# Kernel optimization log

Hardware: AMD Instinct MI355X
Metric: run time of the kernel (lower is better)

The kernel has to match this reference:

```python
import jax, jax.numpy as jnp
import numpy as np

B, T, D, H, HD = 4, 2048, 1024, 16, 64
EPS = 1e-6


def _rotary_tables(seq_len, d_head):
    n = d_head // 4
    angular_freq = (1.0 / 1024) ** jnp.linspace(0, 1, n, dtype=jnp.float32)
    angular_freq = jnp.concatenate([angular_freq, jnp.zeros((n,), jnp.float32)])  # [d_head//2]
    theta = jnp.outer(jnp.arange(seq_len, dtype=jnp.float32), angular_freq)  # [T, d_head//2]
    return jnp.cos(theta), jnp.sin(theta)


def _apply_rotary(x, cos, sin):
    # x: [B, T, H, d]
    xf = x.astype(jnp.float32)
    x1, x2 = jnp.split(xf, 2, axis=-1)
    c = cos[None, :, None, :]
    s = sin[None, :, None, :]
    y1 = x1 * c + x2 * s
    y2 = -x1 * s + x2 * c
    return jnp.concatenate([y1, y2], axis=-1).astype(x.dtype)


def _rmsnorm(x, eps):
    return x * jax.lax.rsqrt(jnp.mean(x * x, axis=-1, keepdims=True) + eps)


def setup_inputs() -> dict:
    key = jax.random.key(0)
    ks = jax.random.split(key, 5)
    scale = 1.0 / np.sqrt(D)
    x = jax.random.normal(ks[0], (B, T, D), jnp.float32)
    wq = jax.random.normal(ks[1], (D, D), jnp.float32) * scale
    wk = jax.random.normal(ks[2], (D, D), jnp.float32) * scale
    wv = jax.random.normal(ks[3], (D, D), jnp.float32) * scale
    wo = jax.random.normal(ks[4], (D, D), jnp.float32) * scale
    mask = jnp.tril(jnp.ones((T, T), dtype=bool))  # causal
    return {"x": x, "wq": wq, "wk": wk, "wv": wv, "wo": wo, "mask": mask}


def reference(x, wq, wk, wv, wo, mask):
    # QKV projections (equinox Linear: y = x @ W.T)
    q = (x @ wq.T).reshape(B, T, H, HD)
    k = (x @ wk.T).reshape(B, T, H, HD)
    v = (x @ wv.T).reshape(B, T, H, HD)
    # QK-norm (RMS norm without weight)
    q = _rmsnorm(q, EPS)
    k = _rmsnorm(k, EPS)
    # Rotary embedding
    cos, sin = _rotary_tables(T, HD)
    q = _apply_rotary(q, cos, sin)
    k = _apply_rotary(k, cos, sin)
    # Attention
    scores = jnp.einsum('bshd,bthd->bhst', q, k) / jnp.sqrt(jnp.float32(HD))
    scores = jnp.where(mask[None, None, :, :], scores, -jnp.inf)
    weights = jax.nn.softmax(scores, axis=-1)
    out = jnp.einsum('bhst,bthd->bshd', weights, v)
    out = out.reshape(B, T, D)
    return out @ wo.T
```

## Files before the change

### kernel.cpp

```cpp
#include <hip/hip_runtime.h>
#include <hip/hip_bf16.h>
#include <math.h>

#define B_ 4
#define T_ 2048
#define D_ 1024
#define H_ 16
#define HD_ 64

typedef _Float16 f16x8 __attribute__((ext_vector_type(8)));
typedef _Float16 f16x4 __attribute__((ext_vector_type(4)));
typedef float f32x4 __attribute__((ext_vector_type(4)));

__device__ __forceinline__ void gload_lds16(const _Float16* g, _Float16* l) {
    __builtin_amdgcn_global_load_lds(
        (const __attribute__((address_space(1))) void*)g,
        (__attribute__((address_space(3))) void*)l,
        16, 0, 0);
}

__global__ __launch_bounds__(256) void castall(const float* __restrict__ x,
                                               const float* __restrict__ wq,
                                               const float* __restrict__ wk,
                                               const float* __restrict__ wv,
                                               const float* __restrict__ wo,
                                               _Float16* __restrict__ xh,
                                               _Float16* __restrict__ wqh,
                                               _Float16* __restrict__ wkh,
                                               _Float16* __restrict__ wvh,
                                               _Float16* __restrict__ woh) {
    const int gi = blockIdx.x * 256 + threadIdx.x;
    const float* in;
    _Float16* out;
    int off;
    if (gi < (1 << 21)) {
        in = x; out = xh; off = gi;
    } else {
        const int j = gi - (1 << 21);
        const int w = j >> 18;
        off = j & ((1 << 18) - 1);
        in  = (w == 0) ? wq : (w == 1 ? wk : (w == 2 ? wv : wo));
        out = (w == 0) ? wqh : (w == 1 ? wkh : (w == 2 ? wvh : woh));
    }
    const float4 v = ((const float4*)in)[off];
    f16x4 h = {(_Float16)v.x, (_Float16)v.y, (_Float16)v.z, (_Float16)v.w};
    ((f16x4*)out)[off] = h;
}

__global__ __launch_bounds__(256) void gemm_qkv(const _Float16* __restrict__ A,
                                                const _Float16* __restrict__ Wq,
                                                const _Float16* __restrict__ Wk,
                                                const _Float16* __restrict__ Wv,
                                                _Float16* __restrict__ qh,
                                                _Float16* __restrict__ kh,
                                                _Float16* __restrict__ vt) {
    constexpr int K = D_;
    const int id  = blockIdx.x + 8 * (blockIdx.y + 64 * blockIdx.z);
    const int nid = (id & 7) * 192 + (id >> 3);
    const int bx  = nid & 7;
    const int rem = nid >> 3;
    const int by  = rem & 63;
    const int z   = rem >> 6;

    const _Float16* W = (z == 0) ? Wq : (z == 1 ? Wk : Wv);
    __shared__ _Float16 As[128 * 32];
    __shared__ _Float16 Bs[128 * 32];
    const int tid = threadIdx.x;
    const int lane = tid & 63, w = tid >> 6;
    const int col = lane & 15, quad = lane >> 4;
    const int wm = w >> 1, wn = w & 1;
    const int row0 = by * 128, col0 = bx * 128;
    const int sr = lane >> 2, sc = (lane & 3) * 8;

    f32x4 acc[4][4];
#pragma unroll
    for (int i = 0; i < 4; ++i)
#pragma unroll
        for (int j = 0; j < 4; ++j) acc[i][j] = (f32x4){0.f, 0.f, 0.f, 0.f};

    for (int kt = 0; kt < K / 32; ++kt) {
        const int k0 = kt * 32;
#pragma unroll
        for (int it = 0; it < 2; ++it) {
            const int rb = it * 64 + w * 16;
            gload_lds16(A + (size_t)(row0 + rb + sr) * K + k0 + sc, As + rb * 32);
            gload_lds16(W + (size_t)(col0 + rb + sr) * K + k0 + sc, Bs + rb * 32);
        }
        __syncthreads();
        f16x8 af[4], bf[4];
#pragma unroll
        for (int i = 0; i < 4; ++i) {
            af[i] = *(const f16x8*)&As[(wm * 64 + i * 16 + col) * 32 + quad * 8];
            bf[i] = *(const f16x8*)&Bs[(wn * 64 + i * 16 + col) * 32 + quad * 8];
        }
#pragma unroll
        for (int mi = 0; mi < 4; ++mi)
#pragma unroll
            for (int ni = 0; ni < 4; ++ni)
                acc[mi][ni] = __builtin_amdgcn_mfma_f32_16x16x32_f16(af[mi], bf[ni],
                                                                     acc[mi][ni], 0, 0, 0);
        __syncthreads();
    }

    if (z < 2) {
        _Float16* C = (z == 0) ? qh : kh;
        const float qscale = (z == 0) ? 0.18033688011112042f : 1.0f;
        const float fr = exp2f(-10.0f * (float)col * (1.0f / 15.0f));
#pragma unroll
        for (int mi = 0; mi < 4; ++mi) {
            float ssq[4];
#pragma unroll
            for (int r = 0; r < 4; ++r) {
                float t = 0.f;
#pragma unroll
                for (int ni = 0; ni < 4; ++ni) t += acc[mi][ni][r] * acc[mi][ni][r];
                ssq[r] = t;
            }
#pragma unroll
            for (int st = 1; st < 16; st <<= 1)
#pragma unroll
                for (int r = 0; r < 4; ++r) ssq[r] += __shfl_xor(ssq[r], st, 64);
            const int rowb = row0 + wm * 64 + mi * 16 + quad * 4;
#pragma unroll
            for (int r = 0; r < 4; ++r) {
                const float scl = rsqrtf(ssq[r] * (1.0f / 64.0f) + 1e-6f) * qscale;
                const int t = (rowb + r) & (T_ - 1);
                float s, c;
                sincosf((float)t * fr, &s, &c);
                const float x0 = acc[mi][0][r] * scl;
                const float x1 = acc[mi][1][r] * scl;
                const float x2 = acc[mi][2][r] * scl;
                const float x3 = acc[mi][3][r] * scl;
                const float y0 = fmaf(x0, c, x2 * s);
                const float y2 = fmaf(x2, c, -x0 * s);
                const size_t base = (size_t)(rowb + r) * D_ + col0 + wn * 64 + col;
                C[base + 0]  = (_Float16)y0;
                C[base + 16] = (_Float16)x1;
                C[base + 32] = (_Float16)y2;
                C[base + 48] = (_Float16)x3;
            }
        }
    } else {
        const int hh = bx * 2 + wn;
#pragma unroll
        for (int mi = 0; mi < 4; ++mi) {
            const int row = row0 + wm * 64 + mi * 16 + quad * 4;
            const int bb = row >> 11;
            const int t0m = row & (T_ - 1);
#pragma unroll
            for (int ni = 0; ni < 4; ++ni) {
                const int d = ni * 16 + col;
                f16x4 pk = {(_Float16)acc[mi][ni][0], (_Float16)acc[mi][ni][1],
                            (_Float16)acc[mi][ni][2], (_Float16)acc[mi][ni][3]};
                *(f16x4*)&vt[((size_t)(bb * H_ + hh) * HD_ + d) * T_ + t0m] = pk;
            }
        }
    }
}

__global__ __launch_bounds__(256) void gemm_wo(const _Float16* __restrict__ A,
                                               const _Float16* __restrict__ W,
                                               float* __restrict__ C) {
    constexpr int K = D_, N = D_;
    const int id  = blockIdx.x + 8 * blockIdx.y;
    const int nid = (id & 7) * 64 + (id >> 3);
    const int bx  = nid & 7;
    const int by  = nid >> 3;

    __shared__ _Float16 As[128 * 32];
    __shared__ _Float16 Bs[128 * 32];
    const int tid = threadIdx.x;
    const int lane = tid & 63, w = tid >> 6;
    const int col = lane & 15, quad = lane >> 4;
    const int wm = w >> 1, wn = w & 1;
    const int row0 = by * 128, col0 = bx * 128;
    const int sr = lane >> 2, sc = (lane & 3) * 8;

    f32x4 acc[4][4];
#pragma unroll
    for (int i = 0; i < 4; ++i)
#pragma unroll
        for (int j = 0; j < 4; ++j) acc[i][j] = (f32x4){0.f, 0.f, 0.f, 0.f};

    for (int kt = 0; kt < K / 32; ++kt) {
        const int k0 = kt * 32;
#pragma unroll
        for (int it = 0; it < 2; ++it) {
            const int rb = it * 64 + w * 16;
            gload_lds16(A + (size_t)(row0 + rb + sr) * K + k0 + sc, As + rb * 32);
            gload_lds16(W + (size_t)(col0 + rb + sr) * K + k0 + sc, Bs + rb * 32);
        }
        __syncthreads();
        f16x8 af[4], bf[4];
#pragma unroll
        for (int i = 0; i < 4; ++i) {
            af[i] = *(const f16x8*)&As[(wm * 64 + i * 16 + col) * 32 + quad * 8];
            bf[i] = *(const f16x8*)&Bs[(wn * 64 + i * 16 + col) * 32 + quad * 8];
        }
#pragma unroll
        for (int mi = 0; mi < 4; ++mi)
#pragma unroll
            for (int ni = 0; ni < 4; ++ni)
                acc[mi][ni] = __builtin_amdgcn_mfma_f32_16x16x32_f16(af[mi], bf[ni],
                                                                     acc[mi][ni], 0, 0, 0);
        __syncthreads();
    }
#pragma unroll
    for (int mi = 0; mi < 4; ++mi)
#pragma unroll
        for (int ni = 0; ni < 4; ++ni)
#pragma unroll
            for (int r = 0; r < 4; ++r)
                C[(size_t)(row0 + wm * 64 + mi * 16 + quad * 4 + r) * N +
                  col0 + wn * 64 + ni * 16 + col] = acc[mi][ni][r];
}

#define LDP 88

__global__ __launch_bounds__(512) void flash_mfma(const _Float16* __restrict__ qh,
                                                  const _Float16* __restrict__ kh,
                                                  const _Float16* __restrict__ vt,
                                                  _Float16* __restrict__ o) {
    __shared__ _Float16 Kl[2][64 * 64];
    __shared__ _Float16 Vl[2][64 * 64];
    __shared__ _Float16 Pl[8][16 * LDP];
    const int tid = threadIdx.x;
    const int lane = tid & 63, w = tid >> 6;
    const int col = lane & 15, quad = lane >> 4;
    const int bh = blockIdx.x, b = bh >> 4, h = bh & 15;
    const int srow = lane >> 3;
    const int schunk = (lane & 7) ^ srow;
    const int sw = col & 7;
    const int rstg = w * 8 + srow;

    const _Float16* kbase = kh + ((size_t)b * T_ * H_ + (size_t)h) * HD_;
    const _Float16* vbase = vt + ((size_t)(b * H_ + h)) * (size_t)HD_ * T_;

    for (int phase = 0; phase < 2; ++phase) {
        const int qt = (phase == 0) ? (int)blockIdx.y : (15 - (int)blockIdx.y);
        const int q0 = qt * 128;

        const int tq = q0 + w * 16 + col;
        const _Float16* qp = qh + ((size_t)(b * T_ + tq) * H_ + h) * HD_ + quad * 8;
        const f16x8 qB0 = *(const f16x8*)(qp);
        const f16x8 qB1 = *(const f16x8*)(qp + 32);

        f32x4 oa[4];
#pragma unroll
        for (int i = 0; i < 4; ++i) oa[i] = (f32x4){0.f, 0.f, 0.f, 0.f};
        float l_ = 0.f;

        const int nkt = 2 * qt + 2;

        gload_lds16(kbase + (size_t)(0 + rstg) * H_ * HD_ + schunk * 8,
                    &Kl[0][(w * 8) * 64]);
        gload_lds16(vbase + (size_t)rstg * T_ + 0 + schunk * 8,
                    &Vl[0][(w * 8) * 64]);
        __builtin_amdgcn_sched_barrier(0);
        asm volatile("s_waitcnt vmcnt(0)" ::: "memory");
        __builtin_amdgcn_sched_barrier(0);
        __builtin_amdgcn_s_barrier();

        for (int kt = 0; kt < nkt; ++kt) {
            const int k0 = kt * 64;
            const int cur = kt & 1;

            if (kt + 1 < nkt) {
                gload_lds16(kbase + (size_t)(k0 + 64 + rstg) * H_ * HD_ + schunk * 8,
                            &Kl[cur ^ 1][(w * 8) * 64]);
                gload_lds16(vbase + (size_t)rstg * T_ + k0 + 64 + schunk * 8,
                            &Vl[cur ^ 1][(w * 8) * 64]);
            }

            f32x4 s[4];
            __builtin_amdgcn_s_setprio(1);
#pragma unroll
            for (int tn = 0; tn < 4; ++tn) {
                const _Float16* kp = &Kl[cur][(tn * 16 + col) * 64];
                const f16x8 kA0 = *(const f16x8*)(kp + ((quad ^ sw) << 3));
                const f16x8 kA1 = *(const f16x8*)(kp + (((quad | 4) ^ sw) << 3));
                f32x4 a = (f32x4){0.f, 0.f, 0.f, 0.f};
                a = __builtin_amdgcn_mfma_f32_16x16x32_f16(kA0, qB0, a, 0, 0, 0);
                a = __builtin_amdgcn_mfma_f32_16x16x32_f16(kA1, qB1, a, 0, 0, 0);
                s[tn] = a;
            }
            __builtin_amdgcn_s_setprio(0);

            if (k0 + 63 > q0 + w * 16) {
                const int qq = q0 + w * 16 + col;
#pragma unroll
                for (int tn = 0; tn < 4; ++tn)
#pragma unroll
                    for (int r = 0; r < 4; ++r) {
                        const int key = k0 + tn * 16 + quad * 4 + r;
                        if (key > qq) s[tn][r] = -1e30f;
                    }
            }

#pragma unroll
            for (int tn = 0; tn < 4; ++tn) {
                f16x4 pk;
#pragma unroll
                for (int r = 0; r < 4; ++r) {
                    const float p = exp2f(s[tn][r]);
                    l_ += p;
                    pk[r] = (_Float16)p;
                }
                *(f16x4*)&Pl[w][col * LDP + tn * 16 + quad * 4] = pk;
            }

            const f16x8 pA0 = *(const f16x8*)&Pl[w][col * LDP + quad * 8];
            const f16x8 pA1 = *(const f16x8*)&Pl[w][col * LDP + quad * 8 + 32];
            __builtin_amdgcn_s_setprio(1);
#pragma unroll
            for (int tn = 0; tn < 4; ++tn) {
                const _Float16* vp = &Vl[cur][(tn * 16 + col) * 64];
                const f16x8 vB0 = *(const f16x8*)(vp + ((quad ^ sw) << 3));
                const f16x8 vB1 = *(const f16x8*)(vp + (((quad | 4) ^ sw) << 3));
                oa[tn] = __builtin_amdgcn_mfma_f32_16x16x32_f16(pA0, vB0, oa[tn], 0, 0, 0);
                oa[tn] = __builtin_amdgcn_mfma_f32_16x16x32_f16(pA1, vB1, oa[tn], 0, 0, 0);
            }
            __builtin_amdgcn_s_setprio(0);

            __builtin_amdgcn_sched_barrier(0);
            asm volatile("s_waitcnt vmcnt(0)" ::: "memory");
            __builtin_amdgcn_sched_barrier(0);
            __builtin_amdgcn_s_barrier();
        }

        l_ += __shfl_xor(l_, 16, 64);
        l_ += __shfl_xor(l_, 32, 64);
        const float linv = 1.0f / l_;
        float inv[4];
#pragma unroll
        for (int r = 0; r < 4; ++r) inv[r] = __shfl(linv, quad * 4 + r, 64);
#pragma unroll
        for (int tn = 0; tn < 4; ++tn)
#pragma unroll
            for (int r = 0; r < 4; ++r)
                o[((size_t)(b * T_ + q0 + w * 16 + quad * 4 + r) * H_ + h) * HD_ + tn * 16 + col] =
                    (_Float16)(oa[tn][r] * inv[r]);
    }
}

extern "C" void kernel_launch(void* const* d_in, const int* in_sizes, int n_in,
                              void* d_out, int out_size, void* d_ws, size_t ws_size,
                              hipStream_t stream) {
    const float* x  = (const float*)d_in[0];
    const float* wq = (const float*)d_in[1];
    const float* wk = (const float*)d_in[2];
    const float* wv = (const float*)d_in[3];
    const float* wo = (const float*)d_in[4];
    float* out = (float*)d_out;

    const size_t NE = (size_t)B_ * T_ * D_;
    const size_t WE = (size_t)D_ * D_;
    _Float16* xh  = (_Float16*)d_ws;
    _Float16* qh  = xh + NE;
    _Float16* kh  = qh + NE;
    _Float16* vth = kh + NE;
    _Float16* oh  = vth + NE;
    _Float16* wqh = oh + NE;
    _Float16* wkh = wqh + WE;
    _Float16* wvh = wkh + WE;
    _Float16* woh = wvh + WE;

    castall<<<12288, 256, 0, stream>>>(x, wq, wk, wv, wo,
                                       xh, wqh, wkh, wvh, woh);

    gemm_qkv<<<dim3(D_ / 128, (B_ * T_) / 128, 3), 256, 0, stream>>>(
        xh, wqh, wkh, wvh, qh, kh, vth);

    flash_mfma<<<dim3(B_ * H_, 8, 1), 512, 0, stream>>>(qh, kh, vth, oh);

    gemm_wo<<<dim3(D_ / 128, (B_ * T_) / 128, 1), 256, 0, stream>>>(oh, woh, out);
}
```

Before: 279.3 us.

## Skip fully masked key tiles per warp, use fast exp2 and packed cvt, drop block swizzle

In the attention loop, each warp now skips the QK, softmax and PV work for key tiles lying entirely above its causal diagonal, while still joining the shared loads and barriers. The exp2f plus scalar half conversion is replaced by the hardware exp2 intrinsic and packed round-toward-zero f16 conversion, which cuts VALU work. Separately, the block-ID remapping in the QKV and output-projection GEMMs is removed in favour of plain grid indices, which may change L2 reuse of the tiles. Using round-toward-zero for P adds a slight precision change.

```diff
diff --git a/kernel.cpp b/kernel.cpp
--- a/kernel.cpp
+++ b/kernel.cpp
@@ -10,6 +10,7 @@
 
 typedef _Float16 f16x8 __attribute__((ext_vector_type(8)));
 typedef _Float16 f16x4 __attribute__((ext_vector_type(4)));
+typedef __fp16 h16x2 __attribute__((ext_vector_type(2)));
 typedef float f32x4 __attribute__((ext_vector_type(4)));
 
 __device__ __forceinline__ void gload_lds16(const _Float16* g, _Float16* l) {
@@ -55,13 +56,7 @@
                                                 _Float16* __restrict__ kh,
                                                 _Float16* __restrict__ vt) {
     constexpr int K = D_;
-    const int id  = blockIdx.x + 8 * (blockIdx.y + 64 * blockIdx.z);
-    const int nid = (id & 7) * 192 + (id >> 3);
-    const int bx  = nid & 7;
-    const int rem = nid >> 3;
-    const int by  = rem & 63;
-    const int z   = rem >> 6;
-
+    const int z = blockIdx.z;
     const _Float16* W = (z == 0) ? Wq : (z == 1 ? Wk : Wv);
     __shared__ _Float16 As[128 * 32];
     __shared__ _Float16 Bs[128 * 32];
@@ -69,7 +64,7 @@
     const int lane = tid & 63, w = tid >> 6;
     const int col = lane & 15, quad = lane >> 4;
     const int wm = w >> 1, wn = w & 1;
-    const int row0 = by * 128, col0 = bx * 128;
+    const int row0 = blockIdx.y * 128, col0 = blockIdx.x * 128;
     const int sr = lane >> 2, sc = (lane & 3) * 8;
 
     f32x4 acc[4][4];
@@ -141,7 +136,7 @@
             }
         }
     } else {
-        const int hh = bx * 2 + wn;
+        const int hh = blockIdx.x * 2 + wn;
 #pragma unroll
         for (int mi = 0; mi < 4; ++mi) {
             const int row = row0 + wm * 64 + mi * 16 + quad * 4;
@@ -162,18 +157,13 @@
                                                const _Float16* __restrict__ W,
                                                float* __restrict__ C) {
     constexpr int K = D_, N = D_;
-    const int id  = blockIdx.x + 8 * blockIdx.y;
-    const int nid = (id & 7) * 64 + (id >> 3);
-    const int bx  = nid & 7;
-    const int by  = nid >> 3;
-
     __shared__ _Float16 As[128 * 32];
     __shared__ _Float16 Bs[128 * 32];
     const int tid = threadIdx.x;
     const int lane = tid & 63, w = tid >> 6;
     const int col = lane & 15, quad = lane >> 4;
     const int wm = w >> 1, wn = w & 1;
-    const int row0 = by * 128, col0 = bx * 128;
+    const int row0 = blockIdx.y * 128, col0 = blockIdx.x * 128;
     const int sr = lane >> 2, sc = (lane & 3) * 8;
 
     f32x4 acc[4][4];
@@ -251,6 +241,7 @@
         float l_ = 0.f;
 
         const int nkt = 2 * qt + 2;
+        const int qmax = q0 + w * 16 + 15;
 
         gload_lds16(kbase + (size_t)(0 + rstg) * H_ * HD_ + schunk * 8,
                     &Kl[0][(w * 8) * 64]);
@@ -272,55 +263,58 @@
                             &Vl[cur ^ 1][(w * 8) * 64]);
             }
 
-            f32x4 s[4];
-            __builtin_amdgcn_s_setprio(1);
-#pragma unroll
-            for (int tn = 0; tn < 4; ++tn) {
-                const _Float16* kp = &Kl[cur][(tn * 16 + col) * 64];
-                const f16x8 kA0 = *(const f16x8*)(kp + ((quad ^ sw) << 3));
-                const f16x8 kA1 = *(const f16x8*)(kp + (((quad | 4) ^ sw) << 3));
-                f32x4 a = (f32x4){0.f, 0.f, 0.f, 0.f};
-                a = __builtin_amdgcn_mfma_f32_16x16x32_f16(kA0, qB0, a, 0, 0, 0);
-                a = __builtin_amdgcn_mfma_f32_16x16x32_f16(kA1, qB1, a, 0, 0, 0);
-                s[tn] = a;
-            }
-            __builtin_amdgcn_s_setprio(0);
-
-            if (k0 + 63 > q0 + w * 16) {
-                const int qq = q0 + w * 16 + col;
-#pragma unroll
-                for (int tn = 0; tn < 4; ++tn)
-#pragma unroll
-                    for (int r = 0; r < 4; ++r) {
-                        const int key = k0 + tn * 16 + quad * 4 + r;
-                        if (key > qq) s[tn][r] = -1e30f;
-                    }
-            }
-
-#pragma unroll
-            for (int tn = 0; tn < 4; ++tn) {
-                f16x4 pk;
-#pragma unroll
-                for (int r = 0; r < 4; ++r) {
-                    const float p = exp2f(s[tn][r]);
-                    l_ += p;
-                    pk[r] = (_Float16)p;
+            if (k0 <= qmax) {
+                f32x4 s[4];
+                __builtin_amdgcn_s_setprio(1);
+#pragma unroll
+                for (int tn = 0; tn < 4; ++tn) {
+                    const _Float16* kp = &Kl[cur][(tn * 16 + col) * 64];
+                    const f16x8 kA0 = *(const f16x8*)(kp + ((quad ^ sw) << 3));
+                    const f16x8 kA1 = *(const f16x8*)(kp + (((quad | 4) ^ sw) << 3));
+                    f32x4 a = (f32x4){0.f, 0.f, 0.f, 0.f};
+                    a = __builtin_amdgcn_mfma_f32_16x16x32_f16(kA0, qB0, a, 0, 0, 0);
+                    a = __builtin_amdgcn_mfma_f32_16x16x32_f16(kA1, qB1, a, 0, 0, 0);
+                    s[tn] = a;
                 }
-                *(f16x4*)&Pl[w][col * LDP + tn * 16 + quad * 4] = pk;
-            }
-
-            const f16x8 pA0 = *(const f16x8*)&Pl[w][col * LDP + quad * 8];
-            const f16x8 pA1 = *(const f16x8*)&Pl[w][col * LDP + quad * 8 + 32];
-            __builtin_amdgcn_s_setprio(1);
-#pragma unroll
-            for (int tn = 0; tn < 4; ++tn) {
-                const _Float16* vp = &Vl[cur][(tn * 16 + col) * 64];
-                const f16x8 vB0 = *(const f16x8*)(vp + ((quad ^ sw) << 3));
-                const f16x8 vB1 = *(const f16x8*)(vp + (((quad | 4) ^ sw) << 3));
-                oa[tn] = __builtin_amdgcn_mfma_f32_16x16x32_f16(pA0, vB0, oa[tn], 0, 0, 0);
-                oa[tn] = __builtin_amdgcn_mfma_f32_16x16x32_f16(pA1, vB1, oa[tn], 0, 0, 0);
-            }
-            __builtin_amdgcn_s_setprio(0);
+                __builtin_amdgcn_s_setprio(0);
+
+                if (k0 + 63 > q0 + w * 16) {
+                    const int qq = q0 + w * 16 + col;
+#pragma unroll
+                    for (int tn = 0; tn < 4; ++tn)
+#pragma unroll
+                        for (int r = 0; r < 4; ++r) {
+                            const int key = k0 + tn * 16 + quad * 4 + r;
+                            if (key > qq) s[tn][r] = -1e30f;
+                        }
+                }
+
+#pragma unroll
+                for (int tn = 0; tn < 4; ++tn) {
+                    float p0 = __builtin_amdgcn_exp2f(s[tn][0]);
+                    float p1 = __builtin_amdgcn_exp2f(s[tn][1]);
+                    float p2 = __builtin_amdgcn_exp2f(s[tn][2]);
+                    float p3 = __builtin_amdgcn_exp2f(s[tn][3]);
+                    l_ += (p0 + p1) + (p2 + p3);
+                    union { f16x4 v; h16x2 h[2]; } u;
+                    u.h[0] = __builtin_amdgcn_cvt_pkrtz(p0, p1);
+                    u.h[1] = __builtin_amdgcn_cvt_pkrtz(p2, p3);
+                    *(f16x4*)&Pl[w][col * LDP + tn * 16 + quad * 4] = u.v;
+                }
+
+                const f16x8 pA0 = *(const f16x8*)&Pl[w][col * LDP + quad * 8];
+                const f16x8 pA1 = *(const f16x8*)&Pl[w][col * LDP + quad * 8 + 32];
+                __builtin_amdgcn_s_setprio(1);
+#pragma unroll
+                for (int tn = 0; tn < 4; ++tn) {
+                    const _Float16* vp = &Vl[cur][(tn * 16 + col) * 64];
+                    const f16x8 vB0 = *(const f16x8*)(vp + ((quad ^ sw) << 3));
+                    const f16x8 vB1 = *(const f16x8*)(vp + (((quad | 4) ^ sw) << 3));
+                    oa[tn] = __builtin_amdgcn_mfma_f32_16x16x32_f16(pA0, vB0, oa[tn], 0, 0, 0);
+                    oa[tn] = __builtin_amdgcn_mfma_f32_16x16x32_f16(pA1, vB1, oa[tn], 0, 0, 0);
+                }
+                __builtin_amdgcn_s_setprio(0);
+            }
 
             __builtin_amdgcn_sched_barrier(0);
             asm volatile("s_waitcnt vmcnt(0)" ::: "memory");
```

Result: faster. 259.5 us (median of 2 runs) (-7.1%).
